# Kernel tuning notes

Hardware: AMD Instinct MI355X
Metric: run time of the kernel (lower is better)

## Reference

```python
import jax, jax.numpy as jnp
import numpy as np

N_EMBD = 1024
N_HEAD = 16
HEAD_DIM = N_EMBD // N_HEAD  # 64
LATENT_DIM = N_EMBD // 2     # 512
B, T = 4, 2048


def setup_inputs() -> dict:
    key = jax.random.key(0)
    ks = jax.random.split(key, 5)
    # weights stored [in, out] so forward is x @ W (equivalent to torch Linear with W.T)
    def init(k, fan_in, fan_out):
        bound = 1.0 / np.sqrt(fan_in)
        return jax.random.uniform(k, (fan_in, fan_out), jnp.float32, -bound, bound)
    return {
        "x": jax.random.normal(ks[0], (B, T, N_EMBD), jnp.float32),
        "Wc_down": init(ks[1], N_EMBD, LATENT_DIM),
        "Wq_up": init(ks[2], LATENT_DIM, N_EMBD),
        "Wkv_up": init(ks[3], LATENT_DIM, 2 * HEAD_DIM),
        "Wc_proj": init(ks[4], N_EMBD, N_EMBD),
    }


def reference(x, Wc_down, Wq_up, Wkv_up, Wc_proj):
    Bsz, Tlen, C = x.shape
    latent = x @ Wc_down                                    # [B,T,latent]
    q = (latent @ Wq_up).reshape(Bsz, Tlen, N_HEAD, HEAD_DIM)  # [B,T,H,D]
    kv = latent @ Wkv_up                                    # [B,T,2D]
    k, v = kv[..., :HEAD_DIM], kv[..., HEAD_DIM:]           # shared across heads (MQA)
    scale = 1.0 / np.sqrt(HEAD_DIM)
    att = jnp.einsum("bthd,bsd->bhts", q, k) * scale        # [B,H,T,T]
    causal = jnp.tril(jnp.ones((Tlen, Tlen), dtype=bool))
    att = jnp.where(causal[None, None], att, -jnp.inf)
    att = jax.nn.softmax(att, axis=-1)
    y = jnp.einsum("bhts,bsd->bthd", att, v).reshape(Bsz, Tlen, C)
    return y @ Wc_proj
```

## Files before the change

kernel.cpp:

```cpp
#include <hip/hip_runtime.h>
#include <hip/hip_bf16.h>


typedef __attribute__((ext_vector_type(8))) short bf16x8;
typedef __attribute__((ext_vector_type(4))) float floatx4;
typedef __attribute__((ext_vector_type(4))) unsigned int uintx4;

#define B_   4
#define T_   2048
#define C_   1024
#define H_   16
#define D_   64
#define L_   512
#define QKV_N 1152

__device__ __forceinline__ float EXP2F(float x) {
    float r;
    asm("v_exp_f32 %0, %1" : "=v"(r) : "v"(x));
    return r;
}

__device__ __forceinline__ unsigned short f2bf(float f) {
    unsigned int x = __float_as_uint(f);
    unsigned int r = (x + 0x7fffu + ((x >> 16) & 1u)) >> 16;
    return (unsigned short)r;
}

__device__ __forceinline__ unsigned int cvtpk_bf(float lo, float hi) {
    unsigned int r;
    asm("v_cvt_pk_bf16_f32 %0, %1, %2" : "=v"(r) : "v"(lo), "v"(hi));
    return r;
}

__device__ __forceinline__ void pl32(unsigned int& d, unsigned int& s) {
    asm("v_permlane32_swap_b32 %0, %1" : "+v"(d), "+v"(s));
}
__device__ __forceinline__ void pl16(unsigned int& d, unsigned int& s) {
    asm("v_permlane16_swap_b32 %0, %1" : "+v"(d), "+v"(s));
}

__device__ __forceinline__ void gload_lds16(const unsigned short* g, char* l) {
    __builtin_amdgcn_global_load_lds(
        (const __attribute__((address_space(1))) void*)g,
        (__attribute__((address_space(3))) void*)l,
        16, 0, 0);
}

__global__ void cvt_bf16(const float* __restrict__ X, unsigned short* __restrict__ Xb, int n4) {
    int i = blockIdx.x * 256 + threadIdx.x;
    if (i >= n4) return;
    float4 v = *(const float4*)(X + (size_t)i * 4);
    ushort4 o;
    o.x = f2bf(v.x); o.y = f2bf(v.y); o.z = f2bf(v.z); o.w = f2bf(v.w);
    *(ushort4*)(Xb + (size_t)i * 4) = o;
}

__global__ void wtrans(const float* __restrict__ W, unsigned short* __restrict__ Wt,
                       int K, int N, float scale) {
    int idx = blockIdx.x * 256 + threadIdx.x;
    if (idx >= K * N) return;
    int n = idx / K, k = idx - n * K;
    Wt[idx] = f2bf(W[(size_t)k * N + n] * scale);
}

__global__ void vtrans(const unsigned short* __restrict__ qkv, unsigned short* __restrict__ Vt) {
    int idx = blockIdx.x * 256 + threadIdx.x;
    int t = idx & (T_ - 1);
    int d = (idx >> 11) & 63;
    int b = idx >> 17;
    Vt[idx] = qkv[((size_t)(b * T_ + t)) * QKV_N + 1024 + 64 + d];
}

#define BM 128
#define BN 128
#define BK 64

template <bool F32OUT>
__global__ __launch_bounds__(256) void gemm_bt(const unsigned short* __restrict__ A,
                                               const unsigned short* __restrict__ Bt,
                                               void* __restrict__ Cout,
                                               int M, int N, int K) {
    __shared__ __align__(16) char ldsA[2][BM * BK * 2];
    __shared__ __align__(16) char ldsB[2][BN * BK * 2];
    const int tid = threadIdx.x;
    const int lane = tid & 63, wave = tid >> 6;
    const int lrow = lane & 15, lhi = lane >> 4;
    const int bm = blockIdx.y * BM, bn = blockIdx.x * BN;
    const int wm = (wave >> 1) * 64, wn = (wave & 1) * 64;

    const unsigned short* ap[4];
    const unsigned short* bp[4];
#pragma unroll
    for (int i = 0; i < 4; ++i) {
        int c = tid + i * 256;
        int row = c >> 3;
        int sc = ((c & 7) ^ (row & 7)) * 8;
        ap[i] = A + (size_t)(bm + row) * K + sc;
        bp[i] = Bt + (size_t)(bn + row) * K + sc;
    }
    const int nk = K >> 6;
    floatx4 acc[4][4] = {};

#pragma unroll
    for (int i = 0; i < 4; ++i) {
        gload_lds16(ap[i], ldsA[0] + (i * 256 + wave * 64) * 16);
        gload_lds16(bp[i], ldsB[0] + (i * 256 + wave * 64) * 16);
        ap[i] += BK; bp[i] += BK;
    }

    for (int t = 0; t < nk; ++t) {
        const int cur = t & 1;
        if (t + 1 < nk) {
#pragma unroll
            for (int i = 0; i < 4; ++i) {
                gload_lds16(ap[i], ldsA[cur ^ 1] + (i * 256 + wave * 64) * 16);
                gload_lds16(bp[i], ldsB[cur ^ 1] + (i * 256 + wave * 64) * 16);
                ap[i] += BK; bp[i] += BK;
            }
            asm volatile("s_waitcnt vmcnt(8)" ::: "memory");
        } else {
            asm volatile("s_waitcnt vmcnt(0)" ::: "memory");
        }
        __builtin_amdgcn_s_barrier();
        __builtin_amdgcn_sched_barrier(0);

#pragma unroll
        for (int kk = 0; kk < 2; ++kk) {
            bf16x8 af[4], bfr[4];
#pragma unroll
            for (int m = 0; m < 4; ++m) {
                int row = wm + m * 16 + lrow;
                int colb = kk * 64 + lhi * 16;
                af[m] = *(const bf16x8*)(ldsA[cur] + row * 128 + (colb ^ ((row & 7) << 4)));
            }
#pragma unroll
            for (int n = 0; n < 4; ++n) {
                int row = wn + n * 16 + lrow;
                int colb = kk * 64 + lhi * 16;
                bfr[n] = *(const bf16x8*)(ldsB[cur] + row * 128 + (colb ^ ((row & 7) << 4)));
            }
#pragma unroll
            for (int m = 0; m < 4; ++m)
#pragma unroll
                for (int n = 0; n < 4; ++n)
                    acc[m][n] = __builtin_amdgcn_mfma_f32_16x16x32_bf16(af[m], bfr[n], acc[m][n], 0, 0, 0);
        }
        __builtin_amdgcn_sched_barrier(0);
        __builtin_amdgcn_s_barrier();
    }
#pragma unroll
    for (int m = 0; m < 4; ++m)
#pragma unroll
        for (int n = 0; n < 4; ++n)
#pragma unroll
            for (int r = 0; r < 4; ++r) {
                int row = bm + wm + m * 16 + lhi * 4 + r;
                int col = bn + wn + n * 16 + lrow;
                float v = acc[m][n][r];
                if (F32OUT)
                    ((float*)Cout)[(size_t)row * N + col] = v;
                else
                    ((unsigned short*)Cout)[(size_t)row * N + col] = f2bf(v);
            }
}

__global__ __launch_bounds__(256, 3) void flash(const unsigned short* __restrict__ QKV,
                                                const unsigned short* __restrict__ Vt,
                                                unsigned short* __restrict__ Y) {
    const int id = blockIdx.x;
    const int qt = 15 - (id >> 6);
    const int h = (id >> 2) & 15;
    const int b = id & 3;
    const int tid = threadIdx.x;
    const int lane = tid & 63, wave = tid >> 6;
    const int lrow = lane & 15, lhi = lane >> 4;

    __shared__ __align__(16) char ldsK[3][64 * 128];
    __shared__ __align__(16) char ldsV[3][64 * 128];

    const int qbase = qt * 128 + wave * 32;
    const unsigned short* KV = QKV + 1024;
    const int nst = qt * 2 + 2;

    const unsigned short* kp[2];
    const unsigned short* vp[2];
#pragma unroll
    for (int i = 0; i < 2; ++i) {
        int c = tid + i * 256;
        int row = c >> 3;
        int sc = ((c & 7) ^ (row & 7)) * 8;
        kp[i] = KV + ((size_t)(b * T_ + row)) * QKV_N + sc;
        vp[i] = Vt + ((size_t)(b * 64 + row)) * T_ + sc;
    }

    bf16x8 qf[2][2];
#pragma unroll
    for (int nf = 0; nf < 2; ++nf)
#pragma unroll
        for (int kk = 0; kk < 2; ++kk) {
            int trow = b * T_ + qbase + nf * 16 + lrow;
            int col = h * 64 + kk * 32 + lhi * 8;
            qf[nf][kk] = *(const bf16x8*)(QKV + (size_t)trow * QKV_N + col);
        }

    floatx4 o[2][4] = {};
    floatx4 ol[2] = {};

    const short one_bf = (short)0x3F80;
    const bf16x8 ones8 = {one_bf, one_bf, one_bf, one_bf, one_bf, one_bf, one_bf, one_bf};

    char* kcur = ldsK[0];  char* kstg = ldsK[1];  char* kfre = ldsK[2];
    char* vcur = ldsV[0];  char* vstg = ldsV[1];  char* vfre = ldsV[2];
#pragma unroll
    for (int i = 0; i < 2; ++i) {
        gload_lds16(kp[i], kcur + (i * 256 + wave * 64) * 16);
        gload_lds16(vp[i], vcur + (i * 256 + wave * 64) * 16);
        kp[i] += 64 * QKV_N;
        vp[i] += 64;
    }

    for (int st = 0; st < nst; ++st) {
        const bool more = (st + 1 < nst);
        const long kadj = more ? 0 : -(long)(64 * QKV_N);
        const long vadj = more ? 0 : -64L;
#pragma unroll
        for (int i = 0; i < 2; ++i) {
            gload_lds16(kp[i] + kadj, kstg + (i * 256 + wave * 64) * 16);
            gload_lds16(vp[i] + vadj, vstg + (i * 256 + wave * 64) * 16);
        }
        if (more) {
            kp[0] += 64 * QKV_N; kp[1] += 64 * QKV_N;
            vp[0] += 64;         vp[1] += 64;
        }
        asm volatile("s_waitcnt vmcnt(4)" ::: "memory");
        __builtin_amdgcn_s_barrier();
        __builtin_amdgcn_sched_barrier(0);

        if (st * 64 <= qbase + 31) {
            floatx4 s[4][2] = {};
#pragma unroll
            for (int kk = 0; kk < 2; ++kk) {
                bf16x8 kf[4];
#pragma unroll
                for (int mf = 0; mf < 4; ++mf) {
                    int row = mf * 16 + lrow;
                    int colb = kk * 64 + lhi * 16;
                    kf[mf] = *(const bf16x8*)(kcur + row * 128 + (colb ^ ((row & 7) << 4)));
                }
                __builtin_amdgcn_s_setprio(1);
#pragma unroll
                for (int mf = 0; mf < 4; ++mf)
#pragma unroll
                    for (int nf = 0; nf < 2; ++nf)
                        s[mf][nf] = __builtin_amdgcn_mfma_f32_16x16x32_bf16(kf[mf], qf[nf][kk], s[mf][nf], 0, 0, 0);
                __builtin_amdgcn_s_setprio(0);
            }

#pragma unroll
            for (int nf = 0; nf < 2; ++nf) {
                if (st * 64 + 63 > qbase + nf * 16) {
                    int qg = qbase + nf * 16 + lrow;
#pragma unroll
                    for (int mf = 0; mf < 4; ++mf)
#pragma unroll
                        for (int r = 0; r < 4; ++r) {
                            int sg = st * 64 + mf * 16 + lhi * 4 + r;
                            if (sg > qg) s[mf][nf][r] = -1e30f;
                        }
                }
#pragma unroll
                for (int mf = 0; mf < 4; ++mf)
#pragma unroll
                    for (int rr = 0; rr < 4; ++rr)
                        s[mf][nf][rr] = EXP2F(s[mf][nf][rr]);
            }

            bf16x8 pfr[2][2];
#pragma unroll
            for (int nf = 0; nf < 2; ++nf)
#pragma unroll
                for (int ss = 0; ss < 2; ++ss) {
                    unsigned int A0 = cvtpk_bf(s[2 * ss][nf][0], s[2 * ss][nf][1]);
                    unsigned int A1 = cvtpk_bf(s[2 * ss][nf][2], s[2 * ss][nf][3]);
                    unsigned int B0 = cvtpk_bf(s[2 * ss + 1][nf][0], s[2 * ss + 1][nf][1]);
                    unsigned int B1 = cvtpk_bf(s[2 * ss + 1][nf][2], s[2 * ss + 1][nf][3]);
                    pl32(A0, B0); pl16(A0, B0);
                    pl32(A1, B1); pl16(A1, B1);
                    uintx4 pw; pw.x = A0; pw.y = A1; pw.z = B0; pw.w = B1;
                    pfr[nf][ss] = __builtin_bit_cast(bf16x8, pw);
                }

#pragma unroll
            for (int ss = 0; ss < 2; ++ss) {
                bf16x8 vf[4];
#pragma unroll
                for (int dn = 0; dn < 4; ++dn) {
                    int row = dn * 16 + lrow;
                    int colb = ss * 64 + lhi * 16;
                    vf[dn] = *(const bf16x8*)(vcur + row * 128 + (colb ^ ((row & 7) << 4)));
                }
                __builtin_amdgcn_s_setprio(1);
#pragma unroll
                for (int m = 0; m < 2; ++m) {
#pragma unroll
                    for (int dn = 0; dn < 4; ++dn)
                        o[m][dn] = __builtin_amdgcn_mfma_f32_16x16x32_bf16(pfr[m][ss], vf[dn], o[m][dn], 0, 0, 0);
                    ol[m] = __builtin_amdgcn_mfma_f32_16x16x32_bf16(pfr[m][ss], ones8, ol[m], 0, 0, 0);
                }
                __builtin_amdgcn_s_setprio(0);
            }
        }

        char* t;
        t = kcur; kcur = kstg; kstg = kfre; kfre = t;
        t = vcur; vcur = vstg; vstg = vfre; vfre = t;
    }

#pragma unroll
    for (int m = 0; m < 2; ++m) {
        float linv[4];
#pragma unroll
        for (int rr = 0; rr < 4; ++rr) linv[rr] = __builtin_amdgcn_rcpf(ol[m][rr]);
#pragma unroll
        for (int dn = 0; dn < 4; ++dn)
#pragma unroll
            for (int rr = 0; rr < 4; ++rr) {
                int trow = b * T_ + qbase + m * 16 + lhi * 4 + rr;
                int col = h * 64 + dn * 16 + lrow;
                Y[(size_t)trow * C_ + col] = f2bf(o[m][dn][rr] * linv[rr]);
            }
    }
}

extern "C" void kernel_launch(void* const* d_in, const int* in_sizes, int n_in,
                              void* d_out, int out_size, void* d_ws, size_t ws_size,
                              hipStream_t stream) {
    (void)in_sizes; (void)n_in; (void)out_size; (void)ws_size;
    const float* x   = (const float*)d_in[0];
    const float* Wd  = (const float*)d_in[1];
    const float* Wq  = (const float*)d_in[2];
    const float* Wkv = (const float*)d_in[3];
    const float* Wp  = (const float*)d_in[4];
    float* out = (float*)d_out;
    char* ws = (char*)d_ws;

    const int BT = B_ * T_;
    const float KSC = 0.125f * 1.44269504f;

    unsigned short* xb     = (unsigned short*)(ws + 0);
    unsigned short* wdT    = (unsigned short*)(ws + 16777216);
    unsigned short* wqkvT  = (unsigned short*)(ws + 17825792);
    unsigned short* wpT    = (unsigned short*)(ws + 19005440);
    unsigned short* latent = (unsigned short*)(ws + 21102592);
    unsigned short* qkv    = (unsigned short*)(ws + 29491200);
    unsigned short* vt     = (unsigned short*)(ws + 48365568);
    unsigned short* yb     = xb;

    cvt_bf16<<<(BT * C_ / 4 + 255) / 256, 256, 0, stream>>>(x, xb, BT * C_ / 4);
    wtrans<<<(C_ * L_ + 255) / 256, 256, 0, stream>>>(Wd, wdT, C_, L_, 1.0f);
    wtrans<<<(L_ * C_ + 255) / 256, 256, 0, stream>>>(Wq, wqkvT, L_, C_, KSC);
    wtrans<<<(L_ * 128 + 255) / 256, 256, 0, stream>>>(Wkv, wqkvT + 1024 * 512, L_, 128, 1.0f);
    wtrans<<<(C_ * C_ + 255) / 256, 256, 0, stream>>>(Wp, wpT, C_, C_, 1.0f);

    gemm_bt<false><<<dim3(L_ / BN, BT / BM), 256, 0, stream>>>(xb, wdT, latent, BT, L_, C_);
    gemm_bt<false><<<dim3(QKV_N / BN, BT / BM), 256, 0, stream>>>(latent, wqkvT, qkv, BT, QKV_N, L_);

    vtrans<<<(B_ * 64 * T_ + 255) / 256, 256, 0, stream>>>(qkv, vt);

    flash<<<1024, 256, 0, stream>>>(qkv, vt, yb);

    gemm_bt<true><<<dim3(C_ / BN, BT / BM), 256, 0, stream>>>(yb, wpT, out, BT, C_, C_);
}
```

Before: 145.4 us.

## Fold down-projection into QKV weights and enlarge flash blocks to 512 threads

Precomputes a combined weight (Wq_up|Wkv_up composed with Wc_down) with a small weight-only GEMM, so activations go through a single x @ Wcomb GEMM instead of two chained GEMMs. The intermediate latent tensor is no longer written or read. The flash kernel now uses 512-thread blocks covering 256 query rows, with each thread loading one K/V chunk per stage. This halves the block count and shares each staged K/V tile across twice as many waves. The costs are a larger activation GEMM (K=1024 instead of 512, minus the first GEMM), different rounding from the bf16 combined weight, and the launch bound changed to 512 threads with a min-blocks hint of 4.

```diff
diff --git a/kernel.cpp b/kernel.cpp
--- a/kernel.cpp
+++ b/kernel.cpp
@@ -164,11 +164,11 @@
             }
 }
 
-__global__ __launch_bounds__(256, 3) void flash(const unsigned short* __restrict__ QKV,
+__global__ __launch_bounds__(512, 4) void flash(const unsigned short* __restrict__ QKV,
                                                 const unsigned short* __restrict__ Vt,
                                                 unsigned short* __restrict__ Y) {
     const int id = blockIdx.x;
-    const int qt = 15 - (id >> 6);
+    const int qt = 7 - (id >> 6);
     const int h = (id >> 2) & 15;
     const int b = id & 3;
     const int tid = threadIdx.x;
@@ -178,19 +178,18 @@
     __shared__ __align__(16) char ldsK[3][64 * 128];
     __shared__ __align__(16) char ldsV[3][64 * 128];
 
-    const int qbase = qt * 128 + wave * 32;
+    const int qbase = qt * 256 + wave * 32;
     const unsigned short* KV = QKV + 1024;
-    const int nst = qt * 2 + 2;
-
-    const unsigned short* kp[2];
-    const unsigned short* vp[2];
-#pragma unroll
-    for (int i = 0; i < 2; ++i) {
-        int c = tid + i * 256;
+    const int nst = qt * 4 + 4;
+
+    const unsigned short* kp;
+    const unsigned short* vp;
+    {
+        int c = tid;
         int row = c >> 3;
         int sc = ((c & 7) ^ (row & 7)) * 8;
-        kp[i] = KV + ((size_t)(b * T_ + row)) * QKV_N + sc;
-        vp[i] = Vt + ((size_t)(b * 64 + row)) * T_ + sc;
+        kp = KV + ((size_t)(b * T_ + row)) * QKV_N + sc;
+        vp = Vt + ((size_t)(b * 64 + row)) * T_ + sc;
     }
 
     bf16x8 qf[2][2];
@@ -211,28 +210,19 @@
 
     char* kcur = ldsK[0];  char* kstg = ldsK[1];  char* kfre = ldsK[2];
     char* vcur = ldsV[0];  char* vstg = ldsV[1];  char* vfre = ldsV[2];
-#pragma unroll
-    for (int i = 0; i < 2; ++i) {
-        gload_lds16(kp[i], kcur + (i * 256 + wave * 64) * 16);
-        gload_lds16(vp[i], vcur + (i * 256 + wave * 64) * 16);
-        kp[i] += 64 * QKV_N;
-        vp[i] += 64;
-    }
+    gload_lds16(kp, kcur + wave * 1024);
+    gload_lds16(vp, vcur + wave * 1024);
+    kp += 64 * QKV_N;
+    vp += 64;
 
     for (int st = 0; st < nst; ++st) {
         const bool more = (st + 1 < nst);
         const long kadj = more ? 0 : -(long)(64 * QKV_N);
         const long vadj = more ? 0 : -64L;
-#pragma unroll
-        for (int i = 0; i < 2; ++i) {
-            gload_lds16(kp[i] + kadj, kstg + (i * 256 + wave * 64) * 16);
-            gload_lds16(vp[i] + vadj, vstg + (i * 256 + wave * 64) * 16);
-        }
-        if (more) {
-            kp[0] += 64 * QKV_N; kp[1] += 64 * QKV_N;
-            vp[0] += 64;         vp[1] += 64;
-        }
-        asm volatile("s_waitcnt vmcnt(4)" ::: "memory");
+        gload_lds16(kp + kadj, kstg + wave * 1024);
+        gload_lds16(vp + vadj, vstg + wave * 1024);
+        if (more) { kp += 64 * QKV_N; vp += 64; }
+        asm volatile("s_waitcnt vmcnt(2)" ::: "memory");
         __builtin_amdgcn_s_barrier();
         __builtin_amdgcn_sched_barrier(0);
 
@@ -348,26 +338,27 @@
     const float KSC = 0.125f * 1.44269504f;
 
     unsigned short* xb     = (unsigned short*)(ws + 0);
-    unsigned short* wdT    = (unsigned short*)(ws + 16777216);
-    unsigned short* wqkvT  = (unsigned short*)(ws + 17825792);
+    unsigned short* wqkvT  = (unsigned short*)(ws + 16777216);
+    unsigned short* wdb    = (unsigned short*)(ws + 17956864);
     unsigned short* wpT    = (unsigned short*)(ws + 19005440);
-    unsigned short* latent = (unsigned short*)(ws + 21102592);
+    unsigned short* wcombT = (unsigned short*)(ws + 21102592);
     unsigned short* qkv    = (unsigned short*)(ws + 29491200);
     unsigned short* vt     = (unsigned short*)(ws + 48365568);
     unsigned short* yb     = xb;
 
     cvt_bf16<<<(BT * C_ / 4 + 255) / 256, 256, 0, stream>>>(x, xb, BT * C_ / 4);
-    wtrans<<<(C_ * L_ + 255) / 256, 256, 0, stream>>>(Wd, wdT, C_, L_, 1.0f);
+    cvt_bf16<<<(C_ * L_ / 4 + 255) / 256, 256, 0, stream>>>(Wd, wdb, C_ * L_ / 4);
     wtrans<<<(L_ * C_ + 255) / 256, 256, 0, stream>>>(Wq, wqkvT, L_, C_, KSC);
     wtrans<<<(L_ * 128 + 255) / 256, 256, 0, stream>>>(Wkv, wqkvT + 1024 * 512, L_, 128, 1.0f);
     wtrans<<<(C_ * C_ + 255) / 256, 256, 0, stream>>>(Wp, wpT, C_, C_, 1.0f);
 
-    gemm_bt<false><<<dim3(L_ / BN, BT / BM), 256, 0, stream>>>(xb, wdT, latent, BT, L_, C_);
-    gemm_bt<false><<<dim3(QKV_N / BN, BT / BM), 256, 0, stream>>>(latent, wqkvT, qkv, BT, QKV_N, L_);
+    gemm_bt<false><<<dim3(C_ / BN, QKV_N / BM), 256, 0, stream>>>(wqkvT, wdb, wcombT, QKV_N, C_, L_);
+
+    gemm_bt<false><<<dim3(QKV_N / BN, BT / BM), 256, 0, stream>>>(xb, wcombT, qkv, BT, QKV_N, C_);
 
     vtrans<<<(B_ * 64 * T_ + 255) / 256, 256, 0, stream>>>(qkv, vt);
 
-    flash<<<1024, 256, 0, stream>>>(qkv, vt, yb);
+    flash<<<512, 512, 0, stream>>>(qkv, vt, yb);
 
     gemm_bt<true><<<dim3(C_ / BN, BT / BM), 256, 0, stream>>>(yb, wpT, out, BT, C_, C_);
 }
```

Result: slower. 173.0 us (+19.0%).
